# Performance work log

Measured on AMD Instinct MI355X. Metric: run time of the kernel, lower is better.

Reference implementation:

```python
import jax, jax.numpy as jnp
import numpy as np


def setup_inputs() -> dict:
    key = jax.random.key(0)
    k1, k2 = jax.random.split(key)
    B = 64
    K = 4096
    latent_shape = (8, 250, 16)
    latent = jax.random.normal(k1, (B,) + latent_shape, dtype=jnp.float32)
    codebook = jax.random.normal(k2, (K,) + latent_shape, dtype=jnp.float32)
    usage_count = jnp.zeros((K,), dtype=jnp.float32)
    return {"latent": latent, "codebook": codebook, "usage_count": usage_count}


def reference(latent, codebook, usage_count):
    B = latent.shape[0]
    K = codebook.shape[0]
    latent_flat = latent.reshape(B, -1).astype(jnp.float32)      # [B, D]
    codebook_flat = codebook.reshape(K, -1).astype(jnp.float32)  # [K, D]

    x2 = jnp.sum(latent_flat * latent_flat, axis=1, keepdims=True)      # [B, 1]
    c2 = jnp.sum(codebook_flat * codebook_flat, axis=1)[None, :]        # [1, K]
    xc = jnp.einsum('bd,kd->bk', latent_flat, codebook_flat)            # [B, K]
    distances = jnp.sqrt(jnp.maximum(x2 + c2 - 2.0 * xc, 0.0))          # [B, K]

    indices = jnp.argmin(distances, axis=1)                             # [B] int
    min_distances = jnp.take_along_axis(distances, indices[:, None], axis=1)[:, 0]

    quantized = codebook[indices].astype(latent.dtype)                  # [B, *latent_shape]

    # scatter-add usage count update (handles duplicate indices)
    new_usage_count = usage_count.at[indices].add(1.0)

    return quantized, indices, min_distances, new_usage_count
```

## Files before the change

kernel.cpp:

```cpp
#include <hip/hip_runtime.h>
#include <math.h>

#define D      32000
#define BNUM   64
#define KNUM   4096
#define DSPLIT 4
#define DPER   (D / DSPLIT)
#define BK     64
#define NK     32
#define KBLKS  (KNUM / NK)
#define STRIDE 68

__global__ __launch_bounds__(256) void dist_gemm(
    const float* __restrict__ latent, const float* __restrict__ codebook,
    float* __restrict__ ws_xc, float* __restrict__ ws_c2)
{
    __shared__ __align__(16) float xs[BNUM * STRIDE];
    __shared__ __align__(16) float cs[NK * STRIDE];

    const int tid = threadIdx.x;
    const int ds  = tid & 7;
    const int kg  = (tid >> 3) & 3;
    const int bg  = tid >> 5;
    const int k0  = blockIdx.x * NK;
    const int d0b = blockIdx.y * DPER;

    float acc[8][8];
#pragma unroll
    for (int i = 0; i < 8; i++)
#pragma unroll
        for (int j = 0; j < 8; j++) acc[i][j] = 0.f;
    float c2a[8] = {0.f, 0.f, 0.f, 0.f, 0.f, 0.f, 0.f, 0.f};

    const int xr = tid >> 2, xc4 = tid & 3;
    const int cr = tid >> 3, cc8 = tid & 7;

    for (int d0 = d0b; d0 < d0b + DPER; d0 += BK) {
        __syncthreads();
#pragma unroll
        for (int q = 0; q < 4; q++) {
            const int col = (q * 4 + xc4) * 4;
            const float4 v = *(const float4*)(latent + (size_t)xr * D + d0 + col);
            *(float4*)(xs + xr * STRIDE + col) = v;
        }
#pragma unroll
        for (int q = 0; q < 2; q++) {
            const int col = (q * 8 + cc8) * 4;
            const float4 v = *(const float4*)(codebook + (size_t)(k0 + cr) * D + d0 + col);
            *(float4*)(cs + cr * STRIDE + col) = v;
        }
        __syncthreads();

#pragma unroll
        for (int t = 0; t < 2; t++) {
            const int dd = 4 * ds + 32 * t;
            float4 cv[8];
#pragma unroll
            for (int j = 0; j < 8; j++)
                cv[j] = *(const float4*)(cs + (kg * 8 + j) * STRIDE + dd);
            if (bg == 0) {
#pragma unroll
                for (int j = 0; j < 8; j++)
                    c2a[j] += cv[j].x * cv[j].x + cv[j].y * cv[j].y +
                              cv[j].z * cv[j].z + cv[j].w * cv[j].w;
            }
#pragma unroll
            for (int i = 0; i < 8; i++) {
                const float4 xv = *(const float4*)(xs + (bg * 8 + i) * STRIDE + dd);
#pragma unroll
                for (int j = 0; j < 8; j++) {
                    acc[i][j] += xv.x * cv[j].x + xv.y * cv[j].y +
                                 xv.z * cv[j].z + xv.w * cv[j].w;
                }
            }
        }
    }

#pragma unroll
    for (int i = 0; i < 8; i++)
#pragma unroll
        for (int j = 0; j < 8; j++) {
            float v = acc[i][j];
            v += __shfl_xor(v, 1);
            v += __shfl_xor(v, 2);
            v += __shfl_xor(v, 4);
            acc[i][j] = v;
        }
    if (ds == 0) {
#pragma unroll
        for (int i = 0; i < 8; i++) {
            float4 w0, w1;
            w0.x = acc[i][0]; w0.y = acc[i][1]; w0.z = acc[i][2]; w0.w = acc[i][3];
            w1.x = acc[i][4]; w1.y = acc[i][5]; w1.z = acc[i][6]; w1.w = acc[i][7];
            const size_t off = ((size_t)blockIdx.y * BNUM + bg * 8 + i) * KNUM + k0 + kg * 8;
            *(float4*)(ws_xc + off)     = w0;
            *(float4*)(ws_xc + off + 4) = w1;
        }
    }
    if (bg == 0) {
#pragma unroll
        for (int j = 0; j < 8; j++) {
            float v = c2a[j];
            v += __shfl_xor(v, 1);
            v += __shfl_xor(v, 2);
            v += __shfl_xor(v, 4);
            if (ds == 0) atomicAdd(ws_c2 + k0 + kg * 8 + j, v);
        }
    }
}

__global__ __launch_bounds__(256) void argmin_k(
    const float* __restrict__ latent, const float* __restrict__ ws_xc,
    const float* __restrict__ ws_c2, const float* __restrict__ usage_in,
    float* __restrict__ out_idx, float* __restrict__ out_mind,
    float* __restrict__ out_usage, int* __restrict__ ws_idx)
{
    const int b = blockIdx.x, tid = threadIdx.x;
    __shared__ float svals[256];
    __shared__ int   sidx[256];

    float s = 0.f;
    const float4* lf4 = (const float4*)(latent + (size_t)b * D);
    for (int i = tid; i < D / 4; i += 256) {
        const float4 v = lf4[i];
        s += v.x * v.x + v.y * v.y + v.z * v.z + v.w * v.w;
    }
    svals[tid] = s;
    __syncthreads();
    for (int off = 128; off > 0; off >>= 1) {
        if (tid < off) svals[tid] += svals[tid + off];
        __syncthreads();
    }
    const float x2 = svals[0];
    __syncthreads();

    float best = 3.402823466e38f;
    int   bi   = 0;
    for (int k = tid; k < KNUM; k += 256) {
        float xc = 0.f;
        for (int sdx = 0; sdx < DSPLIT; sdx++)
            xc += ws_xc[((size_t)sdx * BNUM + b) * KNUM + k];
        const float sc = ws_c2[k] - 2.f * xc;
        if (sc < best) { best = sc; bi = k; }
    }
    svals[tid] = best; sidx[tid] = bi;
    __syncthreads();
    for (int off = 128; off > 0; off >>= 1) {
        if (tid < off) {
            const float ov = svals[tid + off];
            const int   oi = sidx[tid + off];
            if (ov < svals[tid] || (ov == svals[tid] && oi < sidx[tid])) {
                svals[tid] = ov; sidx[tid] = oi;
            }
        }
        __syncthreads();
    }
    if (tid == 0) {
        const int k = sidx[0];
        const float d2 = x2 + svals[0];
        out_mind[b] = sqrtf(fmaxf(d2, 0.f));
        out_idx[b]  = (float)k;
        ws_idx[b]   = k;
    }
    if (tid < 64) out_usage[b * 64 + tid] = usage_in[b * 64 + tid];
}

__global__ __launch_bounds__(256) void gather_k(
    const float* __restrict__ codebook, const int* __restrict__ ws_idx,
    float* __restrict__ out_q, float* __restrict__ out_usage)
{
    const int b = blockIdx.x, tid = threadIdx.x;
    const int k = ws_idx[b];
    const float4* src = (const float4*)(codebook + (size_t)k * D);
    float4*       dst = (float4*)(out_q + (size_t)b * D);
    for (int i = tid; i < D / 4; i += 256) dst[i] = src[i];
    if (tid == 0) atomicAdd(out_usage + k, 1.0f);
}

extern "C" void kernel_launch(void* const* d_in, const int* in_sizes, int n_in,
                              void* d_out, int out_size, void* d_ws, size_t ws_size,
                              hipStream_t stream)
{
    const float* latent   = (const float*)d_in[0];
    const float* codebook = (const float*)d_in[1];
    const float* usage    = (const float*)d_in[2];

    float* out_q     = (float*)d_out;
    float* out_idx   = out_q + (size_t)BNUM * D;
    float* out_mind  = out_idx + BNUM;
    float* out_usage = out_mind + BNUM;

    float* ws_xc  = (float*)d_ws;
    float* ws_c2  = ws_xc + (size_t)DSPLIT * BNUM * KNUM;
    int*   ws_idx = (int*)(ws_c2 + KNUM);

    hipMemsetAsync(ws_c2, 0, KNUM * sizeof(float), stream);
    dist_gemm<<<dim3(KBLKS, DSPLIT), 256, 0, stream>>>(latent, codebook, ws_xc, ws_c2);
    argmin_k<<<BNUM, 256, 0, stream>>>(latent, ws_xc, ws_c2, usage,
                                       out_idx, out_mind, out_usage, ws_idx);
    gather_k<<<BNUM, 256, 0, stream>>>(codebook, ws_idx, out_q, out_usage);
}
```

Baseline: 878.4 us.

## Use split-bf16 MFMA for distance GEMM with register prefetch and wider split-K

Replaces the FP32 scalar-FMA distance GEMM with a matrix-core kernel. Each FP32 operand is split into hi/lo bf16 halves, and three bf16 MFMAs per step approximate FP32 accuracy. Global loads for the next K tile are prefetched into registers while the current tile is computed. The split-K factor goes from 4 to 10 when the workspace is large enough, and the gather kernel is spread over 4 blocks per row. This trades extra conversion work and a slight loss of accuracy, which could flip argmin near-ties, for much higher matrix throughput.

New measurement: 766.0 us. 12.8% less time.

```diff
diff --git a/kernel.cpp b/kernel.cpp
--- a/kernel.cpp
+++ b/kernel.cpp
@@ -4,108 +4,124 @@
 #define D      32000
 #define BNUM   64
 #define KNUM   4096
-#define DSPLIT 4
-#define DPER   (D / DSPLIT)
+#define TN     64
 #define BK     64
-#define NK     32
-#define KBLKS  (KNUM / NK)
-#define STRIDE 68
-
-__global__ __launch_bounds__(256) void dist_gemm(
+#define LDK    72
+
+typedef __attribute__((ext_vector_type(8)))  short  short8;
+typedef __attribute__((ext_vector_type(16))) float  floatx16;
+
+__device__ __forceinline__ unsigned short f32_bf16_rne(float f) {
+    unsigned u = __float_as_uint(f);
+    u += 0x7fff + ((u >> 16) & 1);
+    return (unsigned short)(u >> 16);
+}
+__device__ __forceinline__ float bf16_f32(unsigned short h) {
+    return __uint_as_float(((unsigned)h) << 16);
+}
+
+__global__ __launch_bounds__(256) void dist_mfma(
     const float* __restrict__ latent, const float* __restrict__ codebook,
-    float* __restrict__ ws_xc, float* __restrict__ ws_c2)
-{
-    __shared__ __align__(16) float xs[BNUM * STRIDE];
-    __shared__ __align__(16) float cs[NK * STRIDE];
-
-    const int tid = threadIdx.x;
-    const int ds  = tid & 7;
-    const int kg  = (tid >> 3) & 3;
-    const int bg  = tid >> 5;
-    const int k0  = blockIdx.x * NK;
-    const int d0b = blockIdx.y * DPER;
-
-    float acc[8][8];
-#pragma unroll
-    for (int i = 0; i < 8; i++)
-#pragma unroll
-        for (int j = 0; j < 8; j++) acc[i][j] = 0.f;
-    float c2a[8] = {0.f, 0.f, 0.f, 0.f, 0.f, 0.f, 0.f, 0.f};
-
-    const int xr = tid >> 2, xc4 = tid & 3;
-    const int cr = tid >> 3, cc8 = tid & 7;
-
-    for (int d0 = d0b; d0 < d0b + DPER; d0 += BK) {
-        __syncthreads();
-#pragma unroll
-        for (int q = 0; q < 4; q++) {
-            const int col = (q * 4 + xc4) * 4;
-            const float4 v = *(const float4*)(latent + (size_t)xr * D + d0 + col);
-            *(float4*)(xs + xr * STRIDE + col) = v;
-        }
-#pragma unroll
-        for (int q = 0; q < 2; q++) {
-            const int col = (q * 8 + cc8) * 4;
-            const float4 v = *(const float4*)(codebook + (size_t)(k0 + cr) * D + d0 + col);
-            *(float4*)(cs + cr * STRIDE + col) = v;
-        }
-        __syncthreads();
-
-#pragma unroll
-        for (int t = 0; t < 2; t++) {
-            const int dd = 4 * ds + 32 * t;
-            float4 cv[8];
-#pragma unroll
-            for (int j = 0; j < 8; j++)
-                cv[j] = *(const float4*)(cs + (kg * 8 + j) * STRIDE + dd);
-            if (bg == 0) {
-#pragma unroll
-                for (int j = 0; j < 8; j++)
-                    c2a[j] += cv[j].x * cv[j].x + cv[j].y * cv[j].y +
-                              cv[j].z * cv[j].z + cv[j].w * cv[j].w;
+    float* __restrict__ ws_xc, float* __restrict__ ws_c2, int dper)
+{
+    __shared__ __align__(16) unsigned short xs_hi[BNUM * LDK];
+    __shared__ __align__(16) unsigned short xs_lo[BNUM * LDK];
+    __shared__ __align__(16) unsigned short cs_hi[TN * LDK];
+    __shared__ __align__(16) unsigned short cs_lo[TN * LDK];
+
+    const int tid  = threadIdx.x;
+    const int k0   = blockIdx.x * TN;
+    const int d0b  = blockIdx.y * dper;
+    const int nst  = dper / BK;
+
+    const int col4  = tid & 15;
+    const int rbase = tid >> 4;
+    const float* aptr = latent   + (size_t)rbase * D + d0b + col4 * 4;
+    const float* bptr = codebook + (size_t)(k0 + rbase) * D + d0b + col4 * 4;
+
+    const int wave = tid >> 6, lane = tid & 63;
+    const int lr = lane & 31, lh = lane >> 5;
+    const int mh = (wave & 1) * 32;
+    const int nh = (wave >> 1) * 32;
+    const int aoff = (mh + lr) * LDK + lh * 8;
+    const int boff = (nh + lr) * LDK + lh * 8;
+
+    floatx16 acc;
+#pragma unroll
+    for (int i = 0; i < 16; i++) acc[i] = 0.f;
+    float c2p[4] = {0.f, 0.f, 0.f, 0.f};
+
+    float4 pa[4], pb[4];
+#pragma unroll
+    for (int p = 0; p < 4; p++) {
+        pa[p] = *(const float4*)(aptr + (size_t)(16 * p) * D);
+        pb[p] = *(const float4*)(bptr + (size_t)(16 * p) * D);
+    }
+
+    for (int s = 0; s < nst; ++s) {
+#pragma unroll
+        for (int p = 0; p < 4; p++)
+            c2p[p] += pb[p].x * pb[p].x + pb[p].y * pb[p].y +
+                      pb[p].z * pb[p].z + pb[p].w * pb[p].w;
+
+        __syncthreads();
+#pragma unroll
+        for (int p = 0; p < 4; p++) {
+            const int wo = (rbase + 16 * p) * LDK + col4 * 4;
+            ushort4 h, l;
+            h.x = f32_bf16_rne(pa[p].x); l.x = f32_bf16_rne(pa[p].x - bf16_f32(h.x));
+            h.y = f32_bf16_rne(pa[p].y); l.y = f32_bf16_rne(pa[p].y - bf16_f32(h.y));
+            h.z = f32_bf16_rne(pa[p].z); l.z = f32_bf16_rne(pa[p].z - bf16_f32(h.z));
+            h.w = f32_bf16_rne(pa[p].w); l.w = f32_bf16_rne(pa[p].w - bf16_f32(h.w));
+            *(ushort4*)(xs_hi + wo) = h;
+            *(ushort4*)(xs_lo + wo) = l;
+            h.x = f32_bf16_rne(pb[p].x); l.x = f32_bf16_rne(pb[p].x - bf16_f32(h.x));
+            h.y = f32_bf16_rne(pb[p].y); l.y = f32_bf16_rne(pb[p].y - bf16_f32(h.y));
+            h.z = f32_bf16_rne(pb[p].z); l.z = f32_bf16_rne(pb[p].z - bf16_f32(h.z));
+            h.w = f32_bf16_rne(pb[p].w); l.w = f32_bf16_rne(pb[p].w - bf16_f32(h.w));
+            *(ushort4*)(cs_hi + wo) = h;
+            *(ushort4*)(cs_lo + wo) = l;
+        }
+        __syncthreads();
+
+        if (s + 1 < nst) {
+            const int doff = (s + 1) * BK;
+#pragma unroll
+            for (int p = 0; p < 4; p++) {
+                pa[p] = *(const float4*)(aptr + (size_t)(16 * p) * D + doff);
+                pb[p] = *(const float4*)(bptr + (size_t)(16 * p) * D + doff);
             }
-#pragma unroll
-            for (int i = 0; i < 8; i++) {
-                const float4 xv = *(const float4*)(xs + (bg * 8 + i) * STRIDE + dd);
-#pragma unroll
-                for (int j = 0; j < 8; j++) {
-                    acc[i][j] += xv.x * cv[j].x + xv.y * cv[j].y +
-                                 xv.z * cv[j].z + xv.w * cv[j].w;
-                }
-            }
-        }
-    }
-
-#pragma unroll
-    for (int i = 0; i < 8; i++)
-#pragma unroll
-        for (int j = 0; j < 8; j++) {
-            float v = acc[i][j];
-            v += __shfl_xor(v, 1);
-            v += __shfl_xor(v, 2);
-            v += __shfl_xor(v, 4);
-            acc[i][j] = v;
-        }
-    if (ds == 0) {
-#pragma unroll
-        for (int i = 0; i < 8; i++) {
-            float4 w0, w1;
-            w0.x = acc[i][0]; w0.y = acc[i][1]; w0.z = acc[i][2]; w0.w = acc[i][3];
-            w1.x = acc[i][4]; w1.y = acc[i][5]; w1.z = acc[i][6]; w1.w = acc[i][7];
-            const size_t off = ((size_t)blockIdx.y * BNUM + bg * 8 + i) * KNUM + k0 + kg * 8;
-            *(float4*)(ws_xc + off)     = w0;
-            *(float4*)(ws_xc + off + 4) = w1;
-        }
-    }
-    if (bg == 0) {
-#pragma unroll
-        for (int j = 0; j < 8; j++) {
-            float v = c2a[j];
-            v += __shfl_xor(v, 1);
-            v += __shfl_xor(v, 2);
-            v += __shfl_xor(v, 4);
-            if (ds == 0) atomicAdd(ws_c2 + k0 + kg * 8 + j, v);
-        }
+        }
+
+#pragma unroll
+        for (int ks = 0; ks < 4; ++ks) {
+            const short8 ah = *(const short8*)(xs_hi + aoff + ks * 16);
+            const short8 al = *(const short8*)(xs_lo + aoff + ks * 16);
+            const short8 bh = *(const short8*)(cs_hi + boff + ks * 16);
+            const short8 bl = *(const short8*)(cs_lo + boff + ks * 16);
+            acc = __builtin_amdgcn_mfma_f32_32x32x16_bf16(ah, bh, acc, 0, 0, 0);
+            acc = __builtin_amdgcn_mfma_f32_32x32x16_bf16(ah, bl, acc, 0, 0, 0);
+            acc = __builtin_amdgcn_mfma_f32_32x32x16_bf16(al, bh, acc, 0, 0, 0);
+        }
+    }
+
+    const int split = blockIdx.y;
+#pragma unroll
+    for (int r = 0; r < 16; ++r) {
+        const int row = (r & 3) + 8 * (r >> 2) + 4 * lh;
+        const int b = mh + row;
+        ws_xc[((size_t)split * BNUM + b) * KNUM + (k0 + nh + lr)] = acc[r];
+    }
+
+#pragma unroll
+    for (int p = 0; p < 4; ++p) {
+        float v = c2p[p];
+        v += __shfl_xor(v, 1);
+        v += __shfl_xor(v, 2);
+        v += __shfl_xor(v, 4);
+        v += __shfl_xor(v, 8);
+        if ((lane & 15) == 0)
+            atomicAdd(ws_c2 + k0 + rbase + 16 * p, v);
     }
 }
 
@@ -113,7 +129,7 @@
     const float* __restrict__ latent, const float* __restrict__ ws_xc,
     const float* __restrict__ ws_c2, const float* __restrict__ usage_in,
     float* __restrict__ out_idx, float* __restrict__ out_mind,
-    float* __restrict__ out_usage, int* __restrict__ ws_idx)
+    float* __restrict__ out_usage, int* __restrict__ ws_idx, int dsplit)
 {
     const int b = blockIdx.x, tid = threadIdx.x;
     __shared__ float svals[256];
@@ -138,7 +154,7 @@
     int   bi   = 0;
     for (int k = tid; k < KNUM; k += 256) {
         float xc = 0.f;
-        for (int sdx = 0; sdx < DSPLIT; sdx++)
+        for (int sdx = 0; sdx < dsplit; sdx++)
             xc += ws_xc[((size_t)sdx * BNUM + b) * KNUM + k];
         const float sc = ws_c2[k] - 2.f * xc;
         if (sc < best) { best = sc; bi = k; }
@@ -157,8 +173,7 @@
     }
     if (tid == 0) {
         const int k = sidx[0];
-        const float d2 = x2 + svals[0];
-        out_mind[b] = sqrtf(fmaxf(d2, 0.f));
+        out_mind[b] = sqrtf(fmaxf(x2 + svals[0], 0.f));
         out_idx[b]  = (float)k;
         ws_idx[b]   = k;
     }
@@ -169,12 +184,13 @@
     const float* __restrict__ codebook, const int* __restrict__ ws_idx,
     float* __restrict__ out_q, float* __restrict__ out_usage)
 {
-    const int b = blockIdx.x, tid = threadIdx.x;
+    const int b = blockIdx.x, part = blockIdx.y, tid = threadIdx.x;
     const int k = ws_idx[b];
-    const float4* src = (const float4*)(codebook + (size_t)k * D);
-    float4*       dst = (float4*)(out_q + (size_t)b * D);
-    for (int i = tid; i < D / 4; i += 256) dst[i] = src[i];
-    if (tid == 0) atomicAdd(out_usage + k, 1.0f);
+    const int n4 = D / 4 / 4;
+    const float4* src = (const float4*)(codebook + (size_t)k * D) + part * n4;
+    float4*       dst = (float4*)(out_q + (size_t)b * D) + part * n4;
+    for (int i = tid; i < n4; i += 256) dst[i] = src[i];
+    if (part == 0 && tid == 0) atomicAdd(out_usage + k, 1.0f);
 }
 
 extern "C" void kernel_launch(void* const* d_in, const int* in_sizes, int n_in,
@@ -190,13 +206,17 @@
     float* out_mind  = out_idx + BNUM;
     float* out_usage = out_mind + BNUM;
 
+    int dsplit = 10;
+    if (ws_size < (size_t)dsplit * BNUM * KNUM * 4 + KNUM * 4 + 256) dsplit = 4;
+    const int dper = D / dsplit;
+
     float* ws_xc  = (float*)d_ws;
-    float* ws_c2  = ws_xc + (size_t)DSPLIT * BNUM * KNUM;
+    float* ws_c2  = ws_xc + (size_t)dsplit * BNUM * KNUM;
     int*   ws_idx = (int*)(ws_c2 + KNUM);
 
     hipMemsetAsync(ws_c2, 0, KNUM * sizeof(float), stream);
-    dist_gemm<<<dim3(KBLKS, DSPLIT), 256, 0, stream>>>(latent, codebook, ws_xc, ws_c2);
+    dist_mfma<<<dim3(KNUM / TN, dsplit), 256, 0, stream>>>(latent, codebook, ws_xc, ws_c2, dper);
     argmin_k<<<BNUM, 256, 0, stream>>>(latent, ws_xc, ws_c2, usage,
-                                       out_idx, out_mind, out_usage, ws_idx);
-    gather_k<<<BNUM, 256, 0, stream>>>(codebook, ws_idx, out_q, out_usage);
-}
+                                       out_idx, out_mind, out_usage, ws_idx, dsplit);
+    gather_k<<<dim3(BNUM, 4), 256, 0, stream>>>(codebook, ws_idx, out_q, out_usage);
+}
```
